# Performance work log

Measured on AMD Instinct MI355X. Metric: run time of the kernel, lower is better.

## Reference

```python
import jax, jax.numpy as jnp
import numpy as np

B, S, D = 4, 2048, 768
H = 12
HD = D // H  # 64

def setup_inputs() -> dict:
    key = jax.random.key(0)
    ks = jax.random.split(key, 5)
    scale = 0.02
    return {
        "x": jax.random.normal(ks[0], (B, S, D), dtype=jnp.float32),
        "w_qkv": jax.random.normal(ks[1], (D, 3 * D), dtype=jnp.float32) * scale,
        "b_qkv": jax.random.normal(ks[2], (3 * D,), dtype=jnp.float32) * scale,
        "w_proj": jax.random.normal(ks[3], (D, D), dtype=jnp.float32) * scale,
        "b_proj": jax.random.normal(ks[4], (D,), dtype=jnp.float32) * scale,
    }

def reference(x, w_qkv, b_qkv, w_proj, b_proj):
    bsz, seq_len, dim = x.shape
    qkv = x @ w_qkv + b_qkv                      # [B,S,3D]
    q, k, v = jnp.split(qkv, 3, axis=-1)
    # [B,S,D] -> [B,H,S,HD]
    def heads(t):
        return t.reshape(bsz, seq_len, H, HD).transpose(0, 2, 1, 3)
    q, k, v = heads(q), heads(k), heads(v)
    scores = jnp.einsum('bhqd,bhkd->bhqk', q, k) * (1.0 / np.sqrt(HD))
    causal = jnp.tril(jnp.ones((seq_len, seq_len), dtype=bool))
    scores = jnp.where(causal[None, None], scores, -jnp.inf)
    attn = jax.nn.softmax(scores.astype(jnp.float32), axis=-1).astype(scores.dtype)
    y = jnp.einsum('bhqk,bhkd->bhqd', attn, v)   # [B,H,S,HD]
    y = y.transpose(0, 2, 1, 3).reshape(bsz, seq_len, dim)
    return y @ w_proj + b_proj
```

## Files before the change

kernel.cpp:

```cpp
#include <hip/hip_runtime.h>
#include <hip/hip_bf16.h>
#include <cstdint>

#define BDIM 768
#define HN 12
#define HDIM 64
#define SEQ 2048
#define BATCH 4
#define MTOT (BATCH * SEQ)

typedef __attribute__((ext_vector_type(8))) short bfrag;
typedef __attribute__((ext_vector_type(4))) float f32x4;

union pfu { bfrag f; unsigned u[4]; };

static __device__ __forceinline__ unsigned short f2bf(float f) {
    union { float f; unsigned u; } v; v.f = f;
    unsigned r = v.u + 0x7FFF + ((v.u >> 16) & 1);
    return (unsigned short)(r >> 16);
}

static __device__ __forceinline__ float fexp2(float x) {
    float r; asm("v_exp_f32 %0, %1" : "=v"(r) : "v"(x)); return r;
}

static __device__ __forceinline__ unsigned cvt_pk_bf16(float lo, float hi) {
    unsigned r;
    asm("v_cvt_pk_bf16_f32 %0, %1, %2" : "=v"(r) : "v"(lo), "v"(hi));
    return r;
}

#if __has_builtin(__builtin_amdgcn_permlane32_swap) && __has_builtin(__builtin_amdgcn_permlane16_swap)
#define HAVE_PERMLANE 1
#else
#define HAVE_PERMLANE 0
#endif

static __device__ __forceinline__ float redmax16(float x) {
#if HAVE_PERMLANE
    union { float f; unsigned u; } a; a.f = x;
    auto r = __builtin_amdgcn_permlane16_swap(a.u, a.u, false, false);
    union { unsigned u; float f; } p, q; p.u = r[0]; q.u = r[1];
    return fmaxf(p.f, q.f);
#else
    return fmaxf(x, __shfl_xor(x, 16));
#endif
}

static __device__ __forceinline__ float redmax32(float x) {
#if HAVE_PERMLANE
    union { float f; unsigned u; } a; a.f = x;
    auto r = __builtin_amdgcn_permlane32_swap(a.u, a.u, false, false);
    union { unsigned u; float f; } p, q; p.u = r[0]; q.u = r[1];
    return fmaxf(p.f, q.f);
#else
    return fmaxf(x, __shfl_xor(x, 32));
#endif
}

__global__ __launch_bounds__(256) void conv_f32_bf16(
    const float* __restrict__ in, unsigned short* __restrict__ out, int n8,
    int* __restrict__ qctr)
{
    if (blockIdx.x == 0 && threadIdx.x < 8) qctr[threadIdx.x] = 0;
    const int i = blockIdx.x * 256 + threadIdx.x;
    if (i >= n8) return;
    const float4 a = ((const float4*)in)[i * 2];
    const float4 b = ((const float4*)in)[i * 2 + 1];
    bfrag o;
    o[0] = f2bf(a.x); o[1] = f2bf(a.y); o[2] = f2bf(a.z); o[3] = f2bf(a.w);
    o[4] = f2bf(b.x); o[5] = f2bf(b.y); o[6] = f2bf(b.z); o[7] = f2bf(b.w);
    ((bfrag*)out)[i] = o;
}

__global__ __launch_bounds__(256) void transpose_f32_bf16(
    const float* __restrict__ in, unsigned short* __restrict__ out, int R, int C)
{
    __shared__ unsigned short t[64][72];
    const int tid = threadIdx.x;
    const int c0 = blockIdx.x * 64, r0 = blockIdx.y * 64;
    #pragma unroll
    for (int i = 0; i < 4; ++i) {
        const int r = (tid >> 4) + i * 16;
        const int c = (tid & 15) * 4;
        const float4 v = *(const float4*)&in[(size_t)(r0 + r) * C + c0 + c];
        t[c + 0][r] = f2bf(v.x);
        t[c + 1][r] = f2bf(v.y);
        t[c + 2][r] = f2bf(v.z);
        t[c + 3][r] = f2bf(v.w);
    }
    __syncthreads();
    #pragma unroll
    for (int i = 0; i < 2; ++i) {
        const int c = (tid >> 3) + i * 32;
        const int r = (tid & 7) * 8;
        *(bfrag*)&out[(size_t)(c0 + c) * R + r0 + r] = *(const bfrag*)&t[c][r];
    }
}

__global__ __launch_bounds__(256) void gemm_qkv(
    const unsigned short* __restrict__ A,
    const unsigned short* __restrict__ Bt,
    const float* __restrict__ bias,
    unsigned short* __restrict__ qb,
    unsigned short* __restrict__ kb,
    unsigned short* __restrict__ vTt)
{
    __shared__ unsigned short As[128 * 64];
    __shared__ unsigned short Bs[128 * 64];

    const int tid  = threadIdx.x;
    const int lane = tid & 63;
    const int wid  = tid >> 6;
    const int l15  = lane & 15;
    const int l4   = lane >> 4;
    const int m0 = blockIdx.y * 128;
    const int n0 = blockIdx.x * 128;
    const int wm = (wid >> 1) * 64;
    const int wn = (wid & 1) * 64;

    f32x4 acc[4][4] = {};

    for (int k0 = 0; k0 < BDIM; k0 += 64) {
        __syncthreads();
        #pragma unroll
        for (int i = 0; i < 4; ++i) {
            const int row = wid * 32 + i * 8 + (lane >> 3);
            const int ck  = (((lane & 7) ^ (row & 7)) * 8);
            __builtin_amdgcn_global_load_lds(
                (const __attribute__((address_space(1))) void*)(A + (size_t)(m0 + row) * BDIM + k0 + ck),
                (__attribute__((address_space(3))) void*)(As + (wid * 4 + i) * 512),
                16, 0, 0);
            __builtin_amdgcn_global_load_lds(
                (const __attribute__((address_space(1))) void*)(Bt + (size_t)(n0 + row) * BDIM + k0 + ck),
                (__attribute__((address_space(3))) void*)(Bs + (wid * 4 + i) * 512),
                16, 0, 0);
        }
        __syncthreads();

        #pragma unroll
        for (int ks = 0; ks < 2; ++ks) {
            bfrag af[4], bfv[4];
            #pragma unroll
            for (int mi = 0; mi < 4; ++mi) {
                const int row = wm + mi * 16 + l15;
                const int ch  = (ks * 4 + l4) ^ (row & 7);
                af[mi] = *(const bfrag*)(As + row * 64 + ch * 8);
            }
            #pragma unroll
            for (int ni = 0; ni < 4; ++ni) {
                const int row = wn + ni * 16 + l15;
                const int ch  = (ks * 4 + l4) ^ (row & 7);
                bfv[ni] = *(const bfrag*)(Bs + row * 64 + ch * 8);
            }
            #pragma unroll
            for (int mi = 0; mi < 4; ++mi)
                #pragma unroll
                for (int ni = 0; ni < 4; ++ni)
                    acc[mi][ni] = __builtin_amdgcn_mfma_f32_16x16x32_bf16(
                        af[mi], bfv[ni], acc[mi][ni], 0, 0, 0);
        }
    }

    const int nb = n0 + wn;
    if (nb < 1536) {
        unsigned short* dst = (nb < 768) ? qb : kb;
        const int coff = (nb < 768) ? 0 : 768;
        #pragma unroll
        for (int mi = 0; mi < 4; ++mi)
            #pragma unroll
            for (int ni = 0; ni < 4; ++ni) {
                const int n = nb + ni * 16 + l15;
                const float bv = bias[n];
                #pragma unroll
                for (int r = 0; r < 4; ++r) {
                    const int m = m0 + wm + mi * 16 + l4 * 4 + r;
                    dst[(size_t)m * BDIM + (n - coff)] = f2bf(acc[mi][ni][r] + bv);
                }
            }
    } else {
        #pragma unroll
        for (int mi = 0; mi < 4; ++mi)
            #pragma unroll
            for (int ni = 0; ni < 4; ++ni) {
                const int n = nb + ni * 16 + l15;
                const float bv = bias[n];
                const size_t vrow = (size_t)(m0 >> 11) * 768 + (n - 1536);
                const int mbase = m0 + wm + mi * 16 + l4 * 4;
                const int scol = mbase & (SEQ - 1);
                uint2 u2;
                u2.x = (unsigned)f2bf(acc[mi][ni][0] + bv)
                     | ((unsigned)f2bf(acc[mi][ni][1] + bv) << 16);
                u2.y = (unsigned)f2bf(acc[mi][ni][2] + bv)
                     | ((unsigned)f2bf(acc[mi][ni][3] + bv) << 16);
                *(uint2*)(vTt + vrow * SEQ + scol) = u2;
            }
    }
}

__global__ __launch_bounds__(256) void gemm_proj(
    const unsigned short* __restrict__ A,
    const unsigned short* __restrict__ Bt,
    const float* __restrict__ bias,
    float* __restrict__ C)
{
    __shared__ unsigned short As[64 * 64];
    __shared__ unsigned short Bs[128 * 64];

    const int tid  = threadIdx.x;
    const int lane = tid & 63;
    const int wid  = tid >> 6;
    const int l15  = lane & 15;
    const int l4   = lane >> 4;
    const int m0 = blockIdx.y * 64;
    const int n0 = blockIdx.x * 128;
    const int wm = (wid >> 1) * 32;
    const int wn = (wid & 1) * 64;

    f32x4 acc[2][4] = {};

    for (int k0 = 0; k0 < BDIM; k0 += 64) {
        __syncthreads();
        #pragma unroll
        for (int i = 0; i < 2; ++i) {
            const int row = wid * 16 + i * 8 + (lane >> 3);
            const int ck  = (((lane & 7) ^ (row & 7)) * 8);
            __builtin_amdgcn_global_load_lds(
                (const __attribute__((address_space(1))) void*)(A + (size_t)(m0 + row) * BDIM + k0 + ck),
                (__attribute__((address_space(3))) void*)(As + (wid * 16 + i * 8) * 64),
                16, 0, 0);
        }
        #pragma unroll
        for (int i = 0; i < 4; ++i) {
            const int row = wid * 32 + i * 8 + (lane >> 3);
            const int ck  = (((lane & 7) ^ (row & 7)) * 8);
            __builtin_amdgcn_global_load_lds(
                (const __attribute__((address_space(1))) void*)(Bt + (size_t)(n0 + row) * BDIM + k0 + ck),
                (__attribute__((address_space(3))) void*)(Bs + (wid * 32 + i * 8) * 64),
                16, 0, 0);
        }
        __syncthreads();

        #pragma unroll
        for (int ks = 0; ks < 2; ++ks) {
            bfrag af[2], bfv[4];
            #pragma unroll
            for (int mi = 0; mi < 2; ++mi) {
                const int row = wm + mi * 16 + l15;
                const int ch  = (ks * 4 + l4) ^ (row & 7);
                af[mi] = *(const bfrag*)(As + row * 64 + ch * 8);
            }
            #pragma unroll
            for (int ni = 0; ni < 4; ++ni) {
                const int row = wn + ni * 16 + l15;
                const int ch  = (ks * 4 + l4) ^ (row & 7);
                bfv[ni] = *(const bfrag*)(Bs + row * 64 + ch * 8);
            }
            #pragma unroll
            for (int mi = 0; mi < 2; ++mi)
                #pragma unroll
                for (int ni = 0; ni < 4; ++ni)
                    acc[mi][ni] = __builtin_amdgcn_mfma_f32_16x16x32_bf16(
                        af[mi], bfv[ni], acc[mi][ni], 0, 0, 0);
        }
    }

    #pragma unroll
    for (int mi = 0; mi < 2; ++mi)
        #pragma unroll
        for (int ni = 0; ni < 4; ++ni) {
            const int n = n0 + wn + ni * 16 + l15;
            const float bv = bias[n];
            #pragma unroll
            for (int r = 0; r < 4; ++r) {
                const int m = m0 + wm + mi * 16 + l4 * 4 + r;
                C[(size_t)m * BDIM + n] = acc[mi][ni][r] + bv;
            }
        }
}

#define C2 0.18033688011112042f
#define THR 8.0f

__global__ __launch_bounds__(256, 2) void attn_flash_mfma(
    const unsigned short* __restrict__ qb,
    const unsigned short* __restrict__ kb,
    const unsigned short* __restrict__ vT,
    unsigned short* __restrict__ yatt,
    int* __restrict__ qctr)
{
    __shared__ unsigned short Ks[2][64 * 64];
    __shared__ unsigned short Vs[2][64 * 64];

    const int hint = blockIdx.x & 7;
    const int tid  = threadIdx.x;
    const int lane = tid & 63;
    const int wid  = tid >> 6;
    const int l15  = lane & 15;
    const int l4   = lane >> 4;

    bfrag onesf;
    #pragma unroll
    for (int j = 0; j < 8; ++j) onesf[j] = (short)0x3F80;

    for (;;) {
        __syncthreads();
        if (tid == 0) *(int*)&Ks[0][0] = atomicAdd(&qctr[hint], 1);
        __syncthreads();
        const int it = *(const int*)&Ks[0][0];
        if (it >= 96) break;
        __syncthreads();

        const int bh = hint * 6 + (it % 6);
        const int p  = 15 - (it / 6);
        const int h = bh % HN, b = bh / HN;
        const int q0 = p * 128;
        const int ktmax = 2 * p + 1;

        const unsigned short* kg = kb + (size_t)b * SEQ * BDIM + h * HDIM;
        const unsigned short* vg = vT + (size_t)bh * HDIM * SEQ;

        bfrag qf[2][2];
        {
            const unsigned short* qr0 =
                qb + (size_t)(b * SEQ + q0 + wid * 16 + l15) * BDIM + h * HDIM;
            qf[0][0] = *(const bfrag*)(qr0 + l4 * 8);
            qf[0][1] = *(const bfrag*)(qr0 + 32 + l4 * 8);
            const unsigned short* qr1 = qr0 + (size_t)64 * BDIM;
            qf[1][0] = *(const bfrag*)(qr1 + l4 * 8);
            qf[1][1] = *(const bfrag*)(qr1 + 32 + l4 * 8);
        }

        f32x4 acc0[4] = {}, acc1[4] = {};
        f32x4 accl0 = {}, accl1 = {};
        float m0v = -3.0e38f, m1v = -3.0e38f;

        pfu pf0[2], pf1[2];
        bfrag vr[2][4];
        #pragma unroll
        for (int ks = 0; ks < 2; ++ks) {
            #pragma unroll
            for (int i = 0; i < 4; ++i) { pf0[ks].u[i] = 0u; pf1[ks].u[i] = 0u; }
            #pragma unroll
            for (int ds = 0; ds < 4; ++ds)
                #pragma unroll
                for (int j = 0; j < 8; ++j) vr[ks][ds][j] = 0;
        }

        auto stage = [&](int bufi, int ktile) {
            const int k0 = ktile * 64;
            #pragma unroll
            for (int i = 0; i < 2; ++i) {
                const int row = wid * 16 + i * 8 + (lane >> 3);
                const int ck  = ((lane & 7) ^ (row & 7)) * 8;
                __builtin_amdgcn_global_load_lds(
                    (const __attribute__((address_space(1))) void*)(kg + (size_t)(k0 + row) * BDIM + ck),
                    (__attribute__((address_space(3))) void*)(&Ks[bufi][(wid * 16 + i * 8) * 64]),
                    16, 0, 0);
                __builtin_amdgcn_global_load_lds(
                    (const __attribute__((address_space(1))) void*)(vg + (size_t)row * SEQ + k0 + ck),
                    (__attribute__((address_space(3))) void*)(&Vs[bufi][(wid * 16 + i * 8) * 64]),
                    16, 0, 0);
            }
        };

        auto softmax_dance = [&](f32x4* s, float& mm, pfu* pf, f32x4* acc, f32x4& accl) {
            float mx = s[0][0];
            #pragma unroll
            for (int cs = 0; cs < 4; ++cs)
                #pragma unroll
                for (int r = 0; r < 4; ++r) mx = fmaxf(mx, s[cs][r]);
            mx = redmax16(mx);
            mx = redmax32(mx);
            const float mx2 = mx * C2;

            if (!__all(mx2 <= mm + THR)) {
                const float mnew = fmaxf(mm, mx2);
                const float fac  = fexp2(mm - mnew);
                mm = mnew;
                #pragma unroll
                for (int r = 0; r < 4; ++r) {
                    const float fr = __shfl(fac, (lane & 48) | (l4 * 4 + r));
                    #pragma unroll
                    for (int ds = 0; ds < 4; ++ds) acc[ds][r] *= fr;
                    accl[r] *= fr;
                }
            }

            #pragma unroll
            for (int cs = 0; cs < 4; ++cs)
                #pragma unroll
                for (int r = 0; r < 4; ++r)
                    s[cs][r] = fexp2(fmaf(s[cs][r], C2, -mm));

            unsigned pk[4][2];
            #pragma unroll
            for (int cs = 0; cs < 4; ++cs) {
                pk[cs][0] = cvt_pk_bf16(s[cs][0], s[cs][1]);
                pk[cs][1] = cvt_pk_bf16(s[cs][2], s[cs][3]);
            }
            #pragma unroll
            for (int ks = 0; ks < 2; ++ks)
                #pragma unroll
                for (int i = 0; i < 2; ++i) {
#if HAVE_PERMLANE
                    auto r1 = __builtin_amdgcn_permlane32_swap(
                        pk[ks * 2][i], pk[ks * 2 + 1][i], false, false);
                    auto r2 = __builtin_amdgcn_permlane16_swap(r1[0], r1[1], false, false);
                    pf[ks].u[i]     = r2[0];
                    pf[ks].u[2 + i] = r2[1];
#else
                    const unsigned A  = pk[ks * 2][i];
                    const unsigned B  = pk[ks * 2 + 1][i];
                    const unsigned Ax = __shfl_xor(A, 32);
                    const unsigned Bx = __shfl_xor(B, 32);
                    const unsigned P1 = (l4 < 2) ? A : Bx;
                    const unsigned P2 = (l4 < 2) ? Ax : B;
                    const unsigned S1 = __shfl_xor(P1, 16);
                    const unsigned S2 = __shfl_xor(P2, 16);
                    pf[ks].u[i]     = (l4 & 1) ? S2 : P1;
                    pf[ks].u[2 + i] = (l4 & 1) ? P2 : S1;
#endif
                }
        };

        stage(0, 0);
        __syncthreads();

        int buf = 0;
        for (int kt = 0;;) {
            if (kt < ktmax) stage(buf ^ 1, kt + 1);

            const unsigned short* Kb = Ks[buf];
            const unsigned short* Vb = Vs[buf];

            f32x4 s0[4] = {}, s1[4] = {};
            __builtin_amdgcn_s_setprio(1);
            #pragma unroll
            for (int ks = 0; ks < 2; ++ks) {
                #pragma unroll
                for (int cs = 0; cs < 4; ++cs) {
                    const int row = cs * 16 + l15;
                    const int ch  = (ks * 4 + l4) ^ (row & 7);
                    const bfrag kf = *(const bfrag*)(Kb + row * 64 + ch * 8);
                    s0[cs] = __builtin_amdgcn_mfma_f32_16x16x32_bf16(kf, qf[0][ks], s0[cs], 0, 0, 0);
                    s1[cs] = __builtin_amdgcn_mfma_f32_16x16x32_bf16(kf, qf[1][ks], s1[cs], 0, 0, 0);
                }
            }
            #pragma unroll
            for (int ks = 0; ks < 2; ++ks) {
                #pragma unroll
                for (int ds = 0; ds < 4; ++ds) {
                    acc0[ds] = __builtin_amdgcn_mfma_f32_16x16x32_bf16(pf0[ks].f, vr[ks][ds], acc0[ds], 0, 0, 0);
                    acc1[ds] = __builtin_amdgcn_mfma_f32_16x16x32_bf16(pf1[ks].f, vr[ks][ds], acc1[ds], 0, 0, 0);
                }
                accl0 = __builtin_amdgcn_mfma_f32_16x16x32_bf16(pf0[ks].f, onesf, accl0, 0, 0, 0);
                accl1 = __builtin_amdgcn_mfma_f32_16x16x32_bf16(pf1[ks].f, onesf, accl1, 0, 0, 0);
            }
            __builtin_amdgcn_s_setprio(0);

            #pragma unroll
            for (int ks = 0; ks < 2; ++ks)
                #pragma unroll
                for (int ds = 0; ds < 4; ++ds) {
                    const int vrow = ds * 16 + l15;
                    const int vch  = (ks * 4 + l4) ^ (vrow & 7);
                    vr[ks][ds] = *(const bfrag*)(Vb + vrow * 64 + vch * 8);
                }

            if (kt >= 2 * p) {
                const int qg = q0 + wid * 16 + l15;
                #pragma unroll
                for (int cs = 0; cs < 4; ++cs)
                    #pragma unroll
                    for (int r = 0; r < 4; ++r) {
                        const int kgl = kt * 64 + cs * 16 + l4 * 4 + r;
                        if (kgl > qg)      s0[cs][r] = -3.0e38f;
                        if (kgl > qg + 64) s1[cs][r] = -3.0e38f;
                    }
            }

            softmax_dance(s0, m0v, pf0, acc0, accl0);
            softmax_dance(s1, m1v, pf1, acc1, accl1);

            if (kt == ktmax) break;
            __syncthreads();
            buf ^= 1; ++kt;
        }

        #pragma unroll
        for (int ks = 0; ks < 2; ++ks) {
            #pragma unroll
            for (int ds = 0; ds < 4; ++ds) {
                acc0[ds] = __builtin_amdgcn_mfma_f32_16x16x32_bf16(pf0[ks].f, vr[ks][ds], acc0[ds], 0, 0, 0);
                acc1[ds] = __builtin_amdgcn_mfma_f32_16x16x32_bf16(pf1[ks].f, vr[ks][ds], acc1[ds], 0, 0, 0);
            }
            accl0 = __builtin_amdgcn_mfma_f32_16x16x32_bf16(pf0[ks].f, onesf, accl0, 0, 0, 0);
            accl1 = __builtin_amdgcn_mfma_f32_16x16x32_bf16(pf1[ks].f, onesf, accl1, 0, 0, 0);
        }

        #pragma unroll
        for (int r = 0; r < 4; ++r) {
            const float iv0 = 1.f / accl0[r];
            const float iv1 = 1.f / accl1[r];
            unsigned short* o0 =
                yatt + (size_t)(b * SEQ + q0 + wid * 16 + l4 * 4 + r) * BDIM + h * HDIM;
            unsigned short* o1 = o0 + (size_t)64 * BDIM;
            #pragma unroll
            for (int ds = 0; ds < 4; ++ds) {
                o0[ds * 16 + l15] = f2bf(acc0[ds][r] * iv0);
                o1[ds * 16 + l15] = f2bf(acc1[ds][r] * iv1);
            }
        }
    }
}

extern "C" void kernel_launch(void* const* d_in, const int* in_sizes, int n_in,
                              void* d_out, int out_size, void* d_ws, size_t ws_size,
                              hipStream_t stream)
{
    const float* x      = (const float*)d_in[0];
    const float* w_qkv  = (const float*)d_in[1];
    const float* b_qkv  = (const float*)d_in[2];
    const float* w_proj = (const float*)d_in[3];
    const float* b_proj = (const float*)d_in[4];
    float* out = (float*)d_out;

    unsigned short* xb   = (unsigned short*)d_ws;
    unsigned short* qb   = xb  + (size_t)MTOT * BDIM;
    unsigned short* kbuf = qb  + (size_t)MTOT * BDIM;
    unsigned short* vT   = kbuf + (size_t)MTOT * BDIM;
    unsigned short* yatt = vT  + (size_t)MTOT * BDIM;
    unsigned short* wqT  = yatt + (size_t)MTOT * BDIM;
    unsigned short* wpT  = wqT + (size_t)3 * BDIM * BDIM;
    int*            qctr = (int*)(wpT + (size_t)BDIM * BDIM);

    conv_f32_bf16<<<(MTOT * BDIM / 8 + 255) / 256, 256, 0, stream>>>(
        x, xb, MTOT * BDIM / 8, qctr);
    transpose_f32_bf16<<<dim3(3 * BDIM / 64, BDIM / 64), 256, 0, stream>>>(
        w_qkv, wqT, BDIM, 3 * BDIM);
    transpose_f32_bf16<<<dim3(BDIM / 64, BDIM / 64), 256, 0, stream>>>(
        w_proj, wpT, BDIM, BDIM);

    gemm_qkv<<<dim3(3 * BDIM / 128, MTOT / 128), 256, 0, stream>>>(
        xb, wqT, b_qkv, qb, kbuf, vT);

    attn_flash_mfma<<<dim3(1024), 256, 0, stream>>>(qb, kbuf, vT, yatt, qctr);

    gemm_proj<<<dim3(BDIM / 128, MTOT / 64), 256, 0, stream>>>(
        yatt, wpT, b_proj, out);
}
```

Baseline: 141.6 us.

## Swizzle GEMM workgroup order, tree-reduce softmax max, shrink attention grid

Both GEMMs remap the flat workgroup index with a stride-8 swizzle, so workgroups that run at the same time (likely one per XCD under round-robin dispatch) cover neighbouring tiles and share more data in L2. The per-lane row max in the attention softmax becomes a balanced tree instead of a serial chain, which shortens the dependency chain. The persistent attention kernel, which pulls work from a queue counter, is launched with 640 workgroups instead of 1024, changing occupancy and scheduling. The swizzle relies on the grid size being divisible by 8.

```diff
diff --git a/kernel.cpp b/kernel.cpp
--- a/kernel.cpp
+++ b/kernel.cpp
@@ -114,8 +114,13 @@
     const int wid  = tid >> 6;
     const int l15  = lane & 15;
     const int l4   = lane >> 4;
-    const int m0 = blockIdx.y * 128;
-    const int n0 = blockIdx.x * 128;
+
+    const int nwg  = (int)(gridDim.x * gridDim.y);
+    const int flat = (int)(blockIdx.y * gridDim.x + blockIdx.x);
+    const int swz  = (flat & 7) * (nwg >> 3) + (flat >> 3);
+    const int m0 = (swz / (int)gridDim.x) * 128;
+    const int n0 = (swz % (int)gridDim.x) * 128;
+
     const int wm = (wid >> 1) * 64;
     const int wn = (wid & 1) * 64;
 
@@ -212,8 +217,13 @@
     const int wid  = tid >> 6;
     const int l15  = lane & 15;
     const int l4   = lane >> 4;
-    const int m0 = blockIdx.y * 64;
-    const int n0 = blockIdx.x * 128;
+
+    const int nwg  = (int)(gridDim.x * gridDim.y);
+    const int flat = (int)(blockIdx.y * gridDim.x + blockIdx.x);
+    const int swz  = (flat & 7) * (nwg >> 3) + (flat >> 3);
+    const int m0 = (swz / (int)gridDim.x) * 64;
+    const int n0 = (swz % (int)gridDim.x) * 128;
+
     const int wm = (wid >> 1) * 32;
     const int wn = (wid & 1) * 64;
 
@@ -365,11 +375,18 @@
         };
 
         auto softmax_dance = [&](f32x4* s, float& mm, pfu* pf, f32x4* acc, f32x4& accl) {
-            float mx = s[0][0];
-            #pragma unroll
-            for (int cs = 0; cs < 4; ++cs)
-                #pragma unroll
-                for (int r = 0; r < 4; ++r) mx = fmaxf(mx, s[cs][r]);
+            float t0 = fmaxf(s[0][0], s[0][1]);
+            float t1 = fmaxf(s[0][2], s[0][3]);
+            float t2 = fmaxf(s[1][0], s[1][1]);
+            float t3 = fmaxf(s[1][2], s[1][3]);
+            float t4 = fmaxf(s[2][0], s[2][1]);
+            float t5 = fmaxf(s[2][2], s[2][3]);
+            float t6 = fmaxf(s[3][0], s[3][1]);
+            float t7 = fmaxf(s[3][2], s[3][3]);
+            t0 = fmaxf(t0, t1); t2 = fmaxf(t2, t3);
+            t4 = fmaxf(t4, t5); t6 = fmaxf(t6, t7);
+            t0 = fmaxf(t0, t2); t4 = fmaxf(t4, t6);
+            float mx = fmaxf(t0, t4);
             mx = redmax16(mx);
             mx = redmax32(mx);
             const float mx2 = mx * C2;
@@ -545,7 +562,7 @@
     gemm_qkv<<<dim3(3 * BDIM / 128, MTOT / 128), 256, 0, stream>>>(
         xb, wqT, b_qkv, qb, kbuf, vT);
 
-    attn_flash_mfma<<<dim3(1024), 256, 0, stream>>>(qb, kbuf, vT, yatt, qctr);
+    attn_flash_mfma<<<dim3(640), 256, 0, stream>>>(qb, kbuf, vT, yatt, qctr);
 
     gemm_proj<<<dim3(BDIM / 128, MTOT / 64), 256, 0, stream>>>(
         yatt, wpT, b_proj, out);
```

After: 137.7 us. -2.7%, faster.
